# Optimization experiments

Measured on AMD Instinct MI355X. Metric: run time of the kernel, lower is better.

Reference implementation:

```python
import jax, jax.numpy as jnp
import numpy as np


def conv2d(x, w, b):
    # x: [D, Cin, H, W], w: [Cout, Cin, kh, kw], SAME padding, stride 1
    y = jax.lax.conv_general_dilated(
        x, w, window_strides=(1, 1), padding='SAME',
        dimension_numbers=('NCHW', 'OIHW', 'NCHW'))
    return y + b[None, :, None, None]


def setup_inputs() -> dict:
    key = jax.random.key(0)
    ks = jax.random.split(key, 12)
    B, N, T, H, W = 2, 3, 16, 28, 28
    Cp, Ch, Ck, Cv, Cs = 1024, 512, 64, 512, 256
    s = 0.02
    return {
        'f16': jax.random.normal(ks[0], (B, Cp, H, W), jnp.float32),
        'mk':  jax.random.normal(ks[1], (B, Ck, T, H, W), jnp.float32),
        'mv':  jax.random.normal(ks[2], (B, N, Cv, T, H, W), jnp.float32),
        'h':   jax.random.normal(ks[3], (B, N, Cs, H, W), jnp.float32),
        # KeyProj: 1x1 conv then 3x3 conv
        'w1': jax.random.normal(ks[4], (Ch, Cp, 1, 1), jnp.float32) * s,
        'b1': jnp.zeros((Ch,), jnp.float32),
        'w2': jax.random.normal(ks[5], (Ck, Ch, 3, 3), jnp.float32) * s,
        'b2': jnp.zeros((Ck,), jnp.float32),
        # sensory-updater transform: 3x3 conv, (Cv+Cs) -> 3*Cs
        'wt': jax.random.normal(ks[6], (3 * Cs, Cv + Cs, 3, 3), jnp.float32) * s,
        'bt': jnp.zeros((3 * Cs,), jnp.float32),
    }


def reference(f16, mk, mv, h, w1, b1, w2, b2, wt, bt):
    B, Ck, T = mk.shape[0], mk.shape[1], mk.shape[2]
    N, Cv = mv.shape[1], mv.shape[2]
    Cs = h.shape[2]
    H, W = f16.shape[-2:]
    P = H * W          # query pixels
    M = T * H * W      # memory slots

    # KeyProj: query key from pixel feature
    qk = conv2d(conv2d(f16, w1, b1), w2, b2)          # [B, Ck, H, W]

    # KV-memory affinity read (softmax over memory axis)
    mk_flat = mk.reshape(B, Ck, M)
    qk_flat = qk.reshape(B, Ck, P)
    logits = jnp.einsum('bcm,bcp->bmp', mk_flat, qk_flat) / jnp.sqrt(
        jnp.asarray(Ck, qk.dtype))                     # [B, M, P]
    aff = jax.nn.softmax(logits, axis=1)               # normalize over memory
    readout = jnp.einsum('bncm,bmp->bncp', mv.reshape(B, N, Cv, M), aff)
    readout = readout.reshape(B, N, Cv, H, W)          # [B, N, Cv, H, W]

    # gated recurrent sensory update (recurrent_update)
    x = jnp.concatenate([readout, h], axis=2).reshape(B * N, Cv + Cs, H, W)
    vals = conv2d(x, wt, bt).reshape(B, N, 3 * Cs, H, W)
    forget_g = jax.nn.sigmoid(vals[:, :, :Cs])
    update_g = jax.nn.sigmoid(vals[:, :, Cs:2 * Cs])
    new_vals = jnp.tanh(vals[:, :, 2 * Cs:])
    new_h = forget_g * h * (1.0 - update_g) + update_g * new_vals
    return new_h
```

## Files before the change

### kernel.cpp

```cpp
#include <hip/hip_runtime.h>

typedef unsigned short u16;
typedef unsigned int u32;
typedef float f32x4v __attribute__((ext_vector_type(4)));
typedef __bf16 bf16x8 __attribute__((ext_vector_type(8)));

#define GAS __attribute__((address_space(1)))
#define LAS __attribute__((address_space(3)))

__device__ __forceinline__ u16 f2bf(float f) {
  u32 u = __builtin_bit_cast(u32, f);
  u32 r = (u + 0x7FFFu + ((u >> 16) & 1u)) >> 16;
  return (u16)r;
}
__device__ __forceinline__ float bf2f(u16 h) {
  return __builtin_bit_cast(float, (u32)h << 16);
}
__device__ __forceinline__ void gld_lds16(const void* g, void* l) {
  __builtin_amdgcn_global_load_lds((const GAS void*)g, (LAS void*)l, 16, 0, 0);
}
#define VMCNT(N) asm volatile("s_waitcnt vmcnt(" #N ")" ::: "memory")
#define MFMA16(a, b, c) __builtin_amdgcn_mfma_f32_16x16x32_bf16((a), (b), (c), 0, 0, 0)

template <int CONV>
__device__ __forceinline__ void gemm8p_dev(
    int lb, int Gpad, const u16* A, const u16* B, u16* Cp,
    int M, int N, int Kc, int fullK, int S,
    long strA, long strB, long strC, int Cin, int gx, int gy, int nwg, u16* smem)
{
  const int cpx = Gpad >> 3;
  const int L = (lb & 7) * cpx + (lb >> 3);
  if (L >= nwg) return;
  const int by = L % gy;
  const int rest = L / gy;
  const int bx = rest % gx;
  const int z = rest / gx;

  const int t = threadIdx.x, lane = t & 63, wave = t >> 6;
  const int zb = z / S, s = z - zb * S;
  const int m0 = bx * 256, n0 = by * 256;
  const int kbeg = s * Kc;
  const int kavail = fullK - kbeg;
  const int kc = Kc < kavail ? Kc : kavail;
  const int T = kc >> 6;

  const int srow = t >> 3;
  const int g = ((t & 7) - (srow & 7)) & 7;
  const int ldsoff = t * 8;

  const u16* Asrc[2][2];
  #pragma unroll
  for (int h = 0; h < 2; ++h)
    #pragma unroll
    for (int q = 0; q < 2; ++q) {
      int r = m0 + h * 128 + q * 64 + srow; if (r >= M) r = M - 1;
      Asrc[h][q] = A + (long)zb * strA + (long)r * fullK + kbeg + g * 8;
    }
  const u16* Bsrc[2][2];
  #pragma unroll
  for (int h = 0; h < 2; ++h)
    #pragma unroll
    for (int q = 0; q < 2; ++q) {
      if constexpr (CONV) {
        int pn = n0 + h * 128 + q * 64 + srow; if (pn >= N) pn = 0;
        const int img = pn / 784, p = pn - img * 784;
        const int py = p / 28, px = p - py * 28;
        Bsrc[h][q] = B + ((long)img * 900 + (py + 1) * 30 + (px + 1)) * Cin + g * 8;
      } else {
        int r = n0 + h * 128 + q * 64 + srow; if (r >= N) r = N - 1;
        Bsrc[h][q] = B + (long)zb * strB + (long)r * fullK + kbeg + g * 8;
      }
    }

  auto stageA = [&](int tile, int h) {
    u16* d = smem + (((tile & 1) * 2 + h) * 8192);
    const long ko = (long)tile * 64;
    gld_lds16(Asrc[h][0] + ko, d + ldsoff);
    gld_lds16(Asrc[h][1] + ko, d + 4096 + ldsoff);
  };
  auto stageB = [&](int tile, int h) {
    u16* d = smem + 32768 + (((tile & 1) * 2 + h) * 8192);
    long off;
    if constexpr (CONV) {
      const int kg = kbeg + tile * 64;
      const int tap = kg / Cin, kc2 = kg - tap * Cin;
      off = (long)((tap / 3 - 1) * 30 + (tap % 3 - 1)) * Cin + kc2;
    } else {
      off = (long)tile * 64;
    }
    gld_lds16(Bsrc[h][0] + off, d + ldsoff);
    gld_lds16(Bsrc[h][1] + off, d + 4096 + ldsoff);
  };

  const int wm = wave & 1, wn = wave >> 1;
  const int lr = lane & 15, hi = lane >> 4;
  const int slot0 = ((hi + (lr & 7)) & 7) * 8;
  const int slot1 = (((hi + 4) + (lr & 7)) & 7) * 8;
  f32x4v acc[8][4] = {};
  bf16x8 breg[4][2];

  stageB(0, 0); stageB(0, 1);
  stageA(0, 0); stageA(0, 1);
  stageB(1, 0); stageB(1, 1);
  VMCNT(4);
  __builtin_amdgcn_s_barrier();

  for (int tau = 0; tau < T; ++tau) {
    const int d = tau & 1;
    const u16* aB = smem + ((d * 2 + wm) * 8192);
    const u16* bB = smem + 32768 + ((d * 2 + (wn >> 1)) * 8192);
    const int ta = (tau + 1 < T) ? tau + 1 : T - 1;
    const int tb = (tau + 2 < T) ? tau + 2 : T - 1;
    #pragma unroll
    for (int Q = 0; Q < 4; ++Q) {
      bf16x8 aph[2][2];
      #pragma unroll
      for (int m2 = 0; m2 < 2; ++m2) {
        const int lrow = (Q * 2 + m2) * 16 + lr;
        aph[m2][0] = *(const bf16x8*)&aB[lrow * 64 + slot0];
        aph[m2][1] = *(const bf16x8*)&aB[lrow * 64 + slot1];
      }
      if (Q == 0) {
        #pragma unroll
        for (int n = 0; n < 4; ++n) {
          const int lrow = (wn & 1) * 64 + n * 16 + lr;
          breg[n][0] = *(const bf16x8*)&bB[lrow * 64 + slot0];
          breg[n][1] = *(const bf16x8*)&bB[lrow * 64 + slot1];
        }
      }
      if      (Q == 0) stageA(ta, 0);
      else if (Q == 1) stageA(ta, 1);
      else if (Q == 2) stageB(tb, 0);
      else             { stageB(tb, 1); VMCNT(4); }
      __builtin_amdgcn_sched_barrier(0);
      __builtin_amdgcn_s_barrier();
      __builtin_amdgcn_s_setprio(1);
      #pragma unroll
      for (int m2 = 0; m2 < 2; ++m2)
        #pragma unroll
        for (int n = 0; n < 4; ++n) {
          acc[Q * 2 + m2][n] = MFMA16(aph[m2][0], breg[n][0], acc[Q * 2 + m2][n]);
          acc[Q * 2 + m2][n] = MFMA16(aph[m2][1], breg[n][1], acc[Q * 2 + m2][n]);
        }
      __builtin_amdgcn_s_setprio(0);
      __builtin_amdgcn_sched_barrier(0);
      __builtin_amdgcn_s_barrier();
    }
  }
  VMCNT(0);

  u16* Co = Cp + (long)z * strC;
  #pragma unroll
  for (int m = 0; m < 8; ++m)
    #pragma unroll
    for (int r = 0; r < 4; ++r) {
      const int row = m0 + wm * 128 + m * 16 + hi * 4 + r;
      if (row >= M) continue;
      #pragma unroll
      for (int n = 0; n < 4; ++n) {
        const int col = n0 + wn * 64 + n * 16 + lr;
        if (col < N) Co[(long)row * N + col] = f2bf(acc[m][n][r]);
      }
    }
}

__device__ __forceinline__ void gemmRC_dev(
    int lb, int Gpad, const u16* A, const u16* B, u16* Cp,
    int M, int N, int Kc, int fullK, int S,
    long strA, long strB, long strC, int gx, int gy, int nwg, u16* smem)
{
  const int cpx = Gpad >> 3;
  const int L = (lb & 7) * cpx + (lb >> 3);
  if (L >= nwg) return;
  const int by = L % gy;
  const int rest = L / gy;
  const int bx = rest % gx;
  const int z = rest / gx;

  u16* sA = smem;
  u16* sB = smem + 3 * 8192;
  const int t = threadIdx.x, lane = t & 63, wave = t >> 6;
  const int zb = z / S, s = z - zb * S;
  const int m0 = bx * 256, n0 = by * 128;
  const int kbeg = s * Kc;
  const int niter = Kc >> 5;

  const int schunk = ((t & 3) ^ ((t >> 4) & 3)) * 8;
  const u16* Ap[2]; const u16* Bp;
  #pragma unroll
  for (int q = 0; q < 2; ++q) {
    int ra = m0 + q * 128 + (t >> 2); if (ra >= M) ra = M - 1;
    Ap[q] = A + (long)zb * strA + (long)ra * fullK + schunk;
  }
  {
    int rb = n0 + (t >> 2); if (rb >= N) rb = N - 1;
    Bp = B + (long)zb * strB + (long)rb * fullK + schunk;
  }
  const int ldst = t * 8;

  auto stage = [&](int buf, int kg) {
    u16* dA = sA + buf * 8192;
    gld_lds16(Ap[0] + kg, &dA[ldst]);
    gld_lds16(Ap[1] + kg, &dA[4096 + ldst]);
    gld_lds16(Bp + kg,    &sB[buf * 4096 + ldst]);
  };

  const int wrow = (wave & 3) * 64, wcol = (wave >> 2) * 64;
  const int lr = lane & 15, hi = lane >> 4;
  const int csw = (hi ^ (lr >> 2)) * 8;
  f32x4v acc[4][4] = {};

  for (int p = 0; p < 2 && p < niter; ++p) stage(p, kbeg + p * 32);
  int cur = 0, nxt = 2;
  for (int it = 0; it < niter; ++it) {
    if (it + 2 < niter) {
      stage(nxt, kbeg + (it + 2) * 32);
      VMCNT(6);
    } else {
      const int rem = niter - 1 - it;
      if (rem == 1) VMCNT(3); else VMCNT(0);
    }
    __builtin_amdgcn_s_barrier();
    __builtin_amdgcn_sched_barrier(0);
    const u16* cA = sA + cur * 8192;
    const u16* cB = sB + cur * 4096;
    bf16x8 af[4], bf[4];
    #pragma unroll
    for (int m = 0; m < 4; ++m) af[m] = *(const bf16x8*)&cA[(wrow + m*16 + lr) * 32 + csw];
    #pragma unroll
    for (int n = 0; n < 4; ++n) bf[n] = *(const bf16x8*)&cB[(wcol + n*16 + lr) * 32 + csw];
    __builtin_amdgcn_s_setprio(1);
    #pragma unroll
    for (int m = 0; m < 4; ++m)
      #pragma unroll
      for (int n = 0; n < 4; ++n)
        acc[m][n] = MFMA16(af[m], bf[n], acc[m][n]);
    __builtin_amdgcn_s_setprio(0);
    __builtin_amdgcn_sched_barrier(0);
    __builtin_amdgcn_s_barrier();
    cur = (cur + 1 == 3) ? 0 : cur + 1;
    nxt = (nxt + 1 == 3) ? 0 : nxt + 1;
  }

  u16* Co = Cp + (long)z * strC;
  const int lq = hi * 4;
  #pragma unroll
  for (int m = 0; m < 4; ++m)
    #pragma unroll
    for (int r = 0; r < 4; ++r) {
      const int row = m0 + wrow + m * 16 + lq + r;
      if (row >= M) continue;
      #pragma unroll
      for (int n = 0; n < 4; ++n) {
        const int col = n0 + wcol + n * 16 + lr;
        if (col < N) Co[(long)row * N + col] = f2bf(acc[m][n][r]);
      }
    }
}

__device__ __forceinline__ void border_slot(int slot, int& py, int& px) {
  if (slot < 30)      { py = 0;         px = slot; }
  else if (slot < 60) { py = 29;        px = slot - 30; }
  else if (slot < 88) { py = slot - 59; px = 0; }
  else                { py = slot - 87; px = 29; }
}

__device__ __forceinline__ void transp_dev(
    const float* in, u16* out, int R, int C, int ldOut,
    int bx, int by, int t, float (*tile)[33])
{
  const int c0 = bx * 32, r0 = by * 32;
  const int tx = t & 31, ty = t >> 5;
  for (int i = ty; i < 32; i += 8) {
    const int r = r0 + i, c = c0 + tx;
    tile[i][tx] = (r < R && c < C) ? in[(long)r * C + c] : 0.0f;
  }
  __syncthreads();
  for (int i = ty; i < 32; i += 8) {
    const int r = r0 + tx, c = c0 + i;
    if (c < C && r < R)
      out[(long)c * ldOut + r] = f2bf(tile[tx][i]);
  }
}

__global__ __launch_bounds__(256) void prep1(
    const float* __restrict__ f16, const float* __restrict__ mk,
    const float* __restrict__ w1,
    u16* __restrict__ f16T, u16* __restrict__ mkT, u16* __restrict__ w1b)
{
  __shared__ float tile[32][33];
  const int bid = blockIdx.x, t = threadIdx.x;
  if (bid < 1600) {
    const int bx = bid % 25, by = (bid / 25) % 32, bz = bid / 800;
    transp_dev(f16 + (long)bz * 1024 * 784, f16T + (long)bz * 784 * 1024,
               1024, 784, 1024, bx, by, t, tile);
    return;
  }
  if (bid < 3168) {
    const int lb = bid - 1600;
    const int bx = lb % 392, by = (lb / 392) % 2, bz = lb / 784;
    transp_dev(mk + (long)bz * 64 * 12544, mkT + (long)bz * 12544 * 64,
               64, 12544, 64, bx, by, t, tile);
    return;
  }
  const long i = (long)(bid - 3168) * 256 + t;
  const float4* p = (const float4*)w1 + i * 2;
  const float4 a = p[0], b = p[1];
  u16 o[8] = {f2bf(a.x), f2bf(a.y), f2bf(a.z), f2bf(a.w),
              f2bf(b.x), f2bf(b.y), f2bf(b.z), f2bf(b.w)};
  ((uint4*)w1b)[i] = *(uint4*)o;
}

__global__ __launch_bounds__(512, 4) void fused1(
    const u16* __restrict__ f16T, const u16* __restrict__ w1b, u16* __restrict__ parts,
    const float* __restrict__ mv, u16* __restrict__ mvb,
    const float* __restrict__ w2, u16* __restrict__ w2R,
    const float* __restrict__ wt, u16* __restrict__ wtR,
    u16* __restrict__ out1P)
{
  extern __shared__ u16 smem[];
  const int bid = blockIdx.x, t = threadIdx.x;
  if (bid < 224) {
    gemmRC_dev(bid, 224, f16T, w1b, parts, 1568, 512, 128, 1024, 8,
               0, 0, 1568L * 512, 7, 4, 224, smem);
    return;
  }
  int lb = bid - 224;
  if (lb < 4704) {
    const long g0 = (long)lb * 1024 + t;
    #pragma unroll
    for (int k = 0; k < 2; ++k) {
      const long g = g0 + k * 512;
      const float4* p = (const float4*)mv + g * 2;
      const float4 a = p[0], b = p[1];
      u16 o[8] = {f2bf(a.x), f2bf(a.y), f2bf(a.z), f2bf(a.w),
                  f2bf(b.x), f2bf(b.y), f2bf(b.z), f2bf(b.w)};
      ((uint4*)mvb)[g] = *(uint4*)o;
    }
    return;
  }
  lb -= 4704;
  if (lb < 576) {
    const int idx = lb * 512 + t;
    const int c = idx % 512, tap = (idx / 512) % 9, m = idx / 4608;
    w2R[idx] = f2bf(w2[((long)m * 512 + c) * 9 + tap]);
    return;
  }
  lb -= 576;
  if (lb < 10368) {
    const long idx = (long)lb * 512 + t;
    const int c = (int)(idx % 768), tap = (int)((idx / 768) % 9), m = (int)(idx / 6912);
    wtR[idx] = f2bf(wt[((long)m * 768 + c) * 9 + tap]);
    return;
  }
  lb -= 10368;
  const int gid = lb * 512 + t;
  if (gid < 14848) {
    const int c8 = gid & 63, rest = gid >> 6;
    const int slot = rest % 116, img = rest / 116;
    int py, px; border_slot(slot, py, px);
    *(uint4*)&out1P[((long)img * 900 + py * 30 + px) * 512 + c8 * 8] =
        make_uint4(0, 0, 0, 0);
  }
}

template <int BK>
__global__ __launch_bounds__(256) void gemm_glds(
    const u16* __restrict__ A, const u16* __restrict__ B, u16* __restrict__ C,
    int M, int N, int Kc, int fullK, int S,
    long strA, long strB, long strC, float scale)
{
  constexpr int CPR = BK / 8;
  constexpr int ISS = BK / 16;
  __shared__ u16 sA[2][128 * BK];
  __shared__ u16 sB[2][128 * BK];
  const int t = threadIdx.x, lane = t & 63, wave = t >> 6;
  const int z = blockIdx.z, zb = z / S;
  const int m0 = blockIdx.x * 128, n0 = blockIdx.y * 128;
  const int kbeg = (z - zb * S) * Kc;

  const u16* Aptr[ISS]; const u16* Bptr[ISS]; int lofs[ISS];
  #pragma unroll
  for (int i = 0; i < ISS; ++i) {
    const int tp = i * 256 + t;
    const int r = tp / CPR;
    int c16 = tp % CPR;
    if constexpr (BK == 32) c16 = c16 ^ ((tp >> 4) & 3);
    else                    c16 = (c16 - (r & 7)) & 7;
    int ra = m0 + r; if (ra >= M) ra = M - 1;
    int rb = n0 + r; if (rb >= N) rb = N - 1;
    Aptr[i] = A + (long)zb * strA + (long)ra * fullK + kbeg + c16 * 8;
    Bptr[i] = B + (long)zb * strB + (long)rb * fullK + kbeg + c16 * 8;
    lofs[i] = (i * 256 + (wave << 6)) * 8;
  }
  auto stage = [&](int buf, int k0) {
    #pragma unroll
    for (int i = 0; i < ISS; ++i) {
      gld_lds16(Aptr[i] + k0, &sA[buf][lofs[i]]);
      gld_lds16(Bptr[i] + k0, &sB[buf][lofs[i]]);
    }
  };

  const int wr = (wave >> 1) * 64, wc = (wave & 1) * 64;
  const int lr = lane & 15, hi = lane >> 4;
  f32x4v acc[4][4] = {};
  const int niter = Kc / BK;

  stage(0, 0);
  for (int it = 0; it < niter; ++it) {
    const int cur = it & 1;
    if (it + 1 < niter) {
      stage(cur ^ 1, (it + 1) * BK);
      if constexpr (ISS == 2) VMCNT(4); else VMCNT(8);
    } else {
      VMCNT(0);
    }
    __builtin_amdgcn_s_barrier();
    __builtin_amdgcn_sched_barrier(0);
    #pragma unroll
    for (int kk = 0; kk < BK; kk += 32) {
      bf16x8 af[4], bv[4];
      #pragma unroll
      for (int i = 0; i < 4; ++i) {
        const int row = wr + i*16 + lr;
        int lk;
        if constexpr (BK == 32) lk = kk + ((hi ^ (lr >> 2)) * 8);
        else                    lk = ((((kk >> 3) + hi) + (row & 7)) & 7) * 8;
        af[i] = *(const bf16x8*)&sA[cur][row * BK + lk];
      }
      #pragma unroll
      for (int j = 0; j < 4; ++j) {
        const int row = wc + j*16 + lr;
        int lk;
        if constexpr (BK == 32) lk = kk + ((hi ^ (lr >> 2)) * 8);
        else                    lk = ((((kk >> 3) + hi) + (row & 7)) & 7) * 8;
        bv[j] = *(const bf16x8*)&sB[cur][row * BK + lk];
      }
      __builtin_amdgcn_s_setprio(1);
      #pragma unroll
      for (int i = 0; i < 4; ++i)
        #pragma unroll
        for (int j = 0; j < 4; ++j)
          acc[i][j] = MFMA16(af[i], bv[j], acc[i][j]);
      __builtin_amdgcn_s_setprio(0);
    }
    __builtin_amdgcn_sched_barrier(0);
    __builtin_amdgcn_s_barrier();
  }

  const int lq = hi * 4;
  u16* Cw = C + (long)zb * strC;
  #pragma unroll
  for (int i = 0; i < 4; ++i)
    #pragma unroll
    for (int r = 0; r < 4; ++r) {
      const int row = m0 + wr + i*16 + lq + r;
      if (row >= M) continue;
      #pragma unroll
      for (int j = 0; j < 4; ++j) {
        const int col = n0 + wc + j*16 + lr;
        if (col < N) Cw[(long)row * N + col] = f2bf(acc[i][j][r] * scale);
      }
    }
}

__global__ __launch_bounds__(256) void conv_glds(
    const u16* __restrict__ Wt, const u16* __restrict__ imgP,
    float* __restrict__ Cp, int M, int Cin, int Ntot, int Kc)
{
  __shared__ u16 sA[2][128 * 32];
  __shared__ u16 sB[2][128 * 32];
  const int t = threadIdx.x, lane = t & 63, wave = t >> 6;
  const int z = blockIdx.z;
  const int m0 = blockIdx.x * 128, n0 = blockIdx.y * 128;
  const int kbeg = z * Kc;

  const u16* Aptr[2]; const u16* Bptr[2]; int lofs[2];
  #pragma unroll
  for (int i = 0; i < 2; ++i) {
    const int tp = i * 256 + t;
    const int r = tp >> 2;
    const int c16 = (tp & 3) ^ ((tp >> 4) & 3);
    int ra = m0 + r; if (ra >= M) ra = M - 1;
    int pn = n0 + r; if (pn >= Ntot) pn = 0;
    const int img = pn / 784, p = pn - img * 784;
    const int py = p / 28, px = p - py * 28;
    Aptr[i] = Wt + (long)ra * (9 * Cin) + c16 * 8;
    Bptr[i] = imgP + ((long)img * 900 + (py + 1) * 30 + (px + 1)) * Cin + c16 * 8;
    lofs[i] = (i * 256 + (wave << 6)) * 8;
  }
  auto stage = [&](int buf, int kg) {
    const int tap = kg / Cin, kc = kg - tap * Cin;
    const long off = (long)((tap / 3 - 1) * 30 + (tap % 3 - 1)) * Cin + kc;
    #pragma unroll
    for (int i = 0; i < 2; ++i) {
      gld_lds16(Aptr[i] + kg, &sA[buf][lofs[i]]);
      gld_lds16(Bptr[i] + off, &sB[buf][lofs[i]]);
    }
  };

  const int wr = (wave >> 1) * 64, wc = (wave & 1) * 64;
  const int lr = lane & 15, hi = lane >> 4;
  const int csw = (hi ^ (lr >> 2)) * 8;
  f32x4v acc[4][4] = {};
  const int niter = Kc >> 5;

  stage(0, kbeg);
  for (int it = 0; it < niter; ++it) {
    const int cur = it & 1;
    if (it + 1 < niter) {
      stage(cur ^ 1, kbeg + (it + 1) * 32);
      VMCNT(4);
    } else {
      VMCNT(0);
    }
    __builtin_amdgcn_s_barrier();
    __builtin_amdgcn_sched_barrier(0);
    bf16x8 af[4], bv[4];
    #pragma unroll
    for (int i = 0; i < 4; ++i) af[i] = *(const bf16x8*)&sA[cur][(wr + i*16 + lr) * 32 + csw];
    #pragma unroll
    for (int j = 0; j < 4; ++j) bv[j] = *(const bf16x8*)&sB[cur][(wc + j*16 + lr) * 32 + csw];
    __builtin_amdgcn_s_setprio(1);
    #pragma unroll
    for (int i = 0; i < 4; ++i)
      #pragma unroll
      for (int j = 0; j < 4; ++j)
        acc[i][j] = MFMA16(af[i], bv[j], acc[i][j]);
    __builtin_amdgcn_s_setprio(0);
    __builtin_amdgcn_sched_barrier(0);
    __builtin_amdgcn_s_barrier();
  }

  float* Co = Cp + (long)z * M * Ntot;
  const int lq = hi * 4;
  #pragma unroll
  for (int i = 0; i < 4; ++i)
    #pragma unroll
    for (int r = 0; r < 4; ++r) {
      const int row = m0 + wr + i*16 + lq + r;
      if (row >= M) continue;
      #pragma unroll
      for (int j = 0; j < 4; ++j) {
        const int col = n0 + wc + j*16 + lr;
        if (col < Ntot) Co[(long)row * Ntot + col] = acc[i][j][r];
      }
    }
}

__device__ __forceinline__ void addbf4(float* a, uint2 v) {
  a[0] += bf2f((u16)(v.x & 0xFFFFu));
  a[1] += bf2f((u16)(v.x >> 16));
  a[2] += bf2f((u16)(v.y & 0xFFFFu));
  a[3] += bf2f((u16)(v.y >> 16));
}

__global__ __launch_bounds__(256) void reduce_c1_bf(
    const u16* __restrict__ parts, u16* __restrict__ dst,
    const float* __restrict__ bias, int S)
{
  const long idx = (long)blockIdx.x * 256 + threadIdx.x;
  if (idx >= 1568L * 128) return;
  const int c4 = (int)(idx & 127), p = (int)(idx >> 7);
  const int c = c4 * 4;
  float sum[4] = {bias[c], bias[c+1], bias[c+2], bias[c+3]};
  for (int s = 0; s < S; ++s)
    addbf4(sum, *(const uint2*)&parts[((long)s * 1568 + p) * 512 + c]);
  const int im = p / 784, q = p - im * 784;
  const int qpad = (q / 28 + 1) * 30 + (q % 28 + 1);
  u16 o[4] = {f2bf(sum[0]), f2bf(sum[1]), f2bf(sum[2]), f2bf(sum[3])};
  *(uint2*)&dst[((long)im * 900 + qpad) * 512 + c] = *(uint2*)o;
}

__global__ __launch_bounds__(256) void reduceT_ro(
    const u16* __restrict__ parts, u16* __restrict__ dst, int S)
{
  __shared__ float tile[32][33];
  const int b = blockIdx.z, c0 = blockIdx.x * 32, p0 = blockIdx.y * 32;
  const int tx = threadIdx.x & 31, ty = threadIdx.x >> 5;
  for (int i = ty; i < 32; i += 8) {
    const int pc = min(p0 + tx, 783);
    float s = 0;
    for (int k = 0; k < S; ++k)
      s += bf2f(parts[((long)(b * S + k) * 1536 + c0 + i) * 784 + pc]);
    tile[i][tx] = s;
  }
  __syncthreads();
  for (int i = ty; i < 32; i += 8) {
    const int p = p0 + i, c = c0 + tx;
    if (p < 784) {
      const int n = c >> 9, cc = c & 511;
      const int qpad = (p / 28 + 1) * 30 + (p % 28 + 1);
      dst[((long)(b * 3 + n) * 900 + qpad) * 768 + cc] = f2bf(tile[tx][i]);
    }
  }
}

__global__ __launch_bounds__(256) void reduceT_qk(
    const float* __restrict__ parts, u16* __restrict__ dst,
    const float* __restrict__ bias, int S)
{
  __shared__ float tile[32][33];
  const int b = blockIdx.z, c0 = blockIdx.x * 32, p0 = blockIdx.y * 32;
  const int tx = threadIdx.x & 31, ty = threadIdx.x >> 5;
  for (int i = ty; i < 32; i += 8) {
    const int pc = min(p0 + tx, 783);
    const long base = (long)(c0 + i) * 1568 + b * 784 + pc;
    float s = 0;
    for (int k = 0; k < S; ++k) s += parts[(long)k * 64 * 1568 + base];
    tile[i][tx] = s;
  }
  __syncthreads();
  for (int i = ty; i < 32; i += 8) {
    const int p = p0 + i, c = c0 + tx;
    if (p < 784)
      dst[((long)b * 784 + p) * 64 + c] = f2bf(tile[tx][i] + bias[c]);
  }
}

__global__ __launch_bounds__(256) void softmax_inplace(u16* __restrict__ buf)
{
  uint4* p4 = (uint4*)(buf + (long)blockIdx.x * 12544);
  const int t = threadIdx.x;
  __shared__ float red[4];
  uint4 v[7];
  float mx = -3.0e38f;
  #pragma unroll
  for (int q = 0; q < 7; ++q) {
    const int idx = t + q * 256;
    if (idx < 1568) {
      v[q] = p4[idx];
      const u32 w[4] = {v[q].x, v[q].y, v[q].z, v[q].w};
      #pragma unroll
      for (int e = 0; e < 4; ++e) {
        mx = fmaxf(mx, bf2f((u16)(w[e] & 0xFFFFu)));
        mx = fmaxf(mx, bf2f((u16)(w[e] >> 16)));
      }
    }
  }
  #pragma unroll
  for (int o = 32; o > 0; o >>= 1) mx = fmaxf(mx, __shfl_xor(mx, o));
  if ((t & 63) == 0) red[t >> 6] = mx;
  __syncthreads();
  mx = fmaxf(fmaxf(red[0], red[1]), fmaxf(red[2], red[3]));

  float s = 0.0f;
  #pragma unroll
  for (int q = 0; q < 7; ++q) {
    const int idx = t + q * 256;
    if (idx < 1568) {
      const u32 w[4] = {v[q].x, v[q].y, v[q].z, v[q].w};
      #pragma unroll
      for (int e = 0; e < 4; ++e) {
        s += __expf(bf2f((u16)(w[e] & 0xFFFFu)) - mx);
        s += __expf(bf2f((u16)(w[e] >> 16)) - mx);
      }
    }
  }
  #pragma unroll
  for (int o = 32; o > 0; o >>= 1) s += __shfl_xor(s, o);
  __syncthreads();
  if ((t & 63) == 0) red[t >> 6] = s;
  __syncthreads();
  const float inv = 1.0f / (red[0] + red[1] + red[2] + red[3]);

  #pragma unroll
  for (int q = 0; q < 7; ++q) {
    const int idx = t + q * 256;
    if (idx < 1568) {
      u32 w[4] = {v[q].x, v[q].y, v[q].z, v[q].w};
      #pragma unroll
      for (int e = 0; e < 4; ++e) {
        const float a = __expf(bf2f((u16)(w[e] & 0xFFFFu)) - mx) * inv;
        const float b = __expf(bf2f((u16)(w[e] >> 16)) - mx) * inv;
        w[e] = (u32)f2bf(a) | ((u32)f2bf(b) << 16);
      }
      p4[idx] = make_uint4(w[0], w[1], w[2], w[3]);
    }
  }
}

__global__ __launch_bounds__(512, 2) void fused_ro(
    const u16* __restrict__ mvb, const u16* __restrict__ logaff,
    u16* __restrict__ parts, const float* __restrict__ hin,
    u16* __restrict__ concatP, int Kc, int S)
{
  extern __shared__ u16 smem[];
  const int bid = blockIdx.x, t = threadIdx.x;
  if (bid < 240) {
    gemm8p_dev<0>(bid, 240, mvb, logaff, parts, 1536, 784, Kc, 12544, S,
                  1536L * 12544, 784L * 12544, 1536L * 784, 0, 6, 4, 240, smem);
    return;
  }
  int lb = bid - 240;
  if (lb < 1200) {
    float (*tile)[33] = (float(*)[33])smem;
    const int bx = lb % 8, by = (lb / 8) % 25, zimg = lb / 200;
    const int c0 = bx * 32, p0 = by * 32;
    const int tx = t & 31, ty = t >> 5;
    for (int i = ty; i < 32; i += 16) {
      const int pc = min(p0 + tx, 783);
      tile[i][tx] = hin[((long)zimg * 256 + c0 + i) * 784 + pc];
    }
    __syncthreads();
    for (int i = ty; i < 32; i += 16) {
      const int p = p0 + i, c = c0 + tx;
      if (p < 784) {
        const int qpad = (p / 28 + 1) * 30 + (p % 28 + 1);
        concatP[((long)zimg * 900 + qpad) * 768 + 512 + c] = f2bf(tile[tx][i]);
      }
    }
    return;
  }
  lb -= 1200;
  const int gid = lb * 512 + t;
  if (gid < 66816) {
    const int c8 = gid % 96, rest = gid / 96;
    const int slot = rest % 116, img = rest / 116;
    int py, px; border_slot(slot, py, px);
    *(uint4*)&concatP[((long)img * 900 + py * 30 + px) * 768 + c8 * 8] =
        make_uint4(0, 0, 0, 0);
  }
}

__global__ __launch_bounds__(512, 2) void gemm8p_tr(
    const u16* __restrict__ A, const u16* __restrict__ B, u16* __restrict__ Cp,
    int M, int N, int Kc, int fullK, int S,
    long strC, int Cin, int gx, int gy, int nwg)
{
  extern __shared__ u16 smem[];
  gemm8p_dev<1>(blockIdx.x, (int)gridDim.x, A, B, Cp, M, N, Kc, fullK, S,
                0, 0, strC, Cin, gx, gy, nwg, smem);
}

__global__ __launch_bounds__(256) void treduce_gate(
    const u16* __restrict__ parts, const float* __restrict__ bt,
    const float* __restrict__ h, float* __restrict__ out, int S)
{
  const long i = (long)blockIdx.x * 256 + threadIdx.x;
  if (i >= 6L * 256 * 196) return;
  const int p4 = (int)(i % 196);
  const int rest = (int)(i / 196);
  const int cs = rest % 256, im = rest / 256;
  const long slice = 768L * 4704;
  const long pbase = (long)im * 784 + p4 * 4;
  float F[4] = {}, U[4] = {}, NV[4] = {};
  for (int s = 0; s < S; ++s) {
    const u16* P = parts + (long)s * slice;
    addbf4(F,  *(const uint2*)&P[(long)cs         * 4704 + pbase]);
    addbf4(U,  *(const uint2*)&P[(long)(256 + cs) * 4704 + pbase]);
    addbf4(NV, *(const uint2*)&P[(long)(512 + cs) * 4704 + pbase]);
  }
  const float bF = bt[cs], bU = bt[256 + cs], bN = bt[512 + cs];
  const f32x4v hv = ((const f32x4v*)h)[((long)(im * 256 + cs) * 784 >> 2) + p4];
  f32x4v o;
  #pragma unroll
  for (int q = 0; q < 4; ++q) {
    const float f = F[q] + bF, u = U[q] + bU, nv = NV[q] + bN;
    const float sf = 1.0f / (1.0f + __expf(-f));
    const float su = 1.0f / (1.0f + __expf(-u));
    const float e2 = __expf(2.0f * nv);
    const float tv = (e2 - 1.0f) / (e2 + 1.0f);
    o[q] = sf * hv[q] * (1.0f - su) + su * tv;
  }
  ((f32x4v*)out)[((long)(im * 256 + cs) * 784 >> 2) + p4] = o;
}

__global__ __launch_bounds__(256) void fill_sentinel(float* p, long n) {
  const long i = (long)blockIdx.x * 256 + threadIdx.x;
  if (i < n) p[i] = 12345.0f;
}

extern "C" void kernel_launch(void* const* d_in, const int* in_sizes, int n_in,
                              void* d_out, int out_size, void* d_ws, size_t ws_size,
                              hipStream_t stream) {
  const float* f16 = (const float*)d_in[0];
  const float* mk  = (const float*)d_in[1];
  const float* mv  = (const float*)d_in[2];
  const float* hin = (const float*)d_in[3];
  const float* w1  = (const float*)d_in[4];
  const float* b1  = (const float*)d_in[5];
  const float* w2  = (const float*)d_in[6];
  const float* b2  = (const float*)d_in[7];
  const float* wt  = (const float*)d_in[8];
  const float* bt  = (const float*)d_in[9];
  float* out = (float*)d_out;

  (void)hipFuncSetAttribute((const void*)fused1,
                            hipFuncAttributeMaxDynamicSharedMemorySize, 73728);
  (void)hipFuncSetAttribute((const void*)fused_ro,
                            hipFuncAttributeMaxDynamicSharedMemorySize, 131072);
  (void)hipFuncSetAttribute((const void*)gemm8p_tr,
                            hipFuncAttributeMaxDynamicSharedMemorySize, 131072);
  constexpr unsigned DSMR = 73728, DSM8 = 131072;

  const size_t B_f16T   = 2UL*784*1024*2;
  const size_t B_w1b    = 512UL*1024*2;
  const size_t B_w2R    = 64UL*4608*2;
  const size_t B_out1P  = 2UL*900*512*2;
  const size_t B_qkT    = 2UL*784*64*2;
  const size_t B_concat = 6UL*900*768*2;
  const size_t B_wtR    = 768UL*6912*2;
  const size_t B_mkT    = 2UL*12544*64*2;
  const size_t B_logaff = 2UL*784*12544*2;
  const size_t B_mvb    = 38535168UL*2;
  auto al = [](size_t x) { return (x + 255) & ~(size_t)255; };

  const size_t phase1 = al(B_f16T) + al(B_w1b) + al(B_w2R) + al(B_out1P) + al(B_qkT);
  const size_t regionA = phase1 > al(B_concat) ? phase1 : al(B_concat);

  const int S_ro = 5, S_tr = 4, S_c1 = 8;
  const int Kc_ro = 2560, Kc_tr = 1728;
  auto poolBytes = [&]() -> size_t {
    size_t p2 = 18UL*64*1568*4;
    size_t p1 = (size_t)S_c1*1568*512*2;
    size_t pr = (size_t)(2*S_ro)*1536*784*2;
    size_t pt = (size_t)S_tr*768*4704*2;
    size_t m = p2; if (p1 > m) m = p1; if (pr > m) m = pr; if (pt > m) m = pt;
    return m;
  };
  const size_t fixed = regionA + al(B_wtR) + al(B_mkT) + al(B_logaff) + al(B_mvb);
  if (fixed + poolBytes() > ws_size) {
    fill_sentinel<<<4704, 256, 0, stream>>>(out, (long)out_size);
    return;
  }

  char* base = (char*)d_ws;
  size_t off = 0;
  auto alloc = [&](size_t bytes) -> char* { char* p = base + off; off += al(bytes); return p; };
  char* rA = alloc(regionA);
  u16* f16T   = (u16*)rA;
  u16* w1b    = (u16*)(rA + al(B_f16T));
  u16* w2R    = (u16*)(rA + al(B_f16T) + al(B_w1b));
  u16* out1P  = (u16*)(rA + al(B_f16T) + al(B_w1b) + al(B_w2R));
  u16* qkT    = (u16*)(rA + al(B_f16T) + al(B_w1b) + al(B_w2R) + al(B_out1P));
  u16* concatP = (u16*)rA;
  u16*   wtR     = (u16*)alloc(B_wtR);
  u16*   mkT     = (u16*)alloc(B_mkT);
  u16*   logaff  = (u16*)alloc(B_logaff);
  u16*   mvb     = (u16*)alloc(B_mvb);
  char*  partsRaw = alloc(poolBytes());
  float* partsF  = (float*)partsRaw;
  u16*   partsH  = (u16*)partsRaw;

  prep1<<<3424, 256, 0, stream>>>(f16, mk, w1, f16T, mkT, w1b);

  fused1<<<15901, 512, DSMR, stream>>>(f16T, w1b, partsH, mv, mvb,
                                       w2, w2R, wt, wtR, out1P);

  reduce_c1_bf<<<784, 256, 0, stream>>>(partsH, out1P, b1, S_c1);

  conv_glds<<<dim3(1, 13, 18), 256, 0, stream>>>(w2R, out1P, partsF, 64, 512, 1568, 256);

  reduceT_qk<<<dim3(2, 25, 2), 256, 0, stream>>>(partsF, qkT, b2, 18);

  gemm_glds<64><<<dim3(7, 98, 2), 256, 0, stream>>>(
      qkT, mkT, logaff, 784, 12544, 64, 64, 1,
      784L*64, 12544L*64, 784L*12544, 0.125f);

  softmax_inplace<<<1568, 256, 0, stream>>>(logaff);

  fused_ro<<<1571, 512, DSM8, stream>>>(mvb, logaff, partsH, hin, concatP,
                                        Kc_ro, S_ro);

  reduceT_ro<<<dim3(48, 25, 2), 256, 0, stream>>>(partsH, concatP, S_ro);

  gemm8p_tr<<<232, 512, DSM8, stream>>>(wtR, concatP, partsH,
                                        768, 4704, Kc_tr, 6912, S_tr,
                                        768L*4704, 768, 3, 19, 228);

  treduce_gate<<<1176, 256, 0, stream>>>(partsH, bt, hin, out, S_tr);
}
```

Before: 305.8 us.

## Rebalance conversion work across kernels to overlap with conv and GEMM

Moves the w2/wt weight reorder-and-convert out of fused1 into prep1, and moves the large mv fp32-to-bf16 conversion into a new conv2_mv kernel that runs it alongside the small 3x3 conv GEMM. fused1 now holds only the 1x1 conv GEMM and border zeroing, so its GEMM blocks no longer share the launch with thousands of elementwise blocks. The aim is to fill idle CUs during the underoccupied conv (234 blocks) with bandwidth-bound conversion work. The risk is that the conversion blocks compete with the conv for bandwidth, and prep1 gets larger.

```diff
diff --git a/kernel.cpp b/kernel.cpp
--- a/kernel.cpp
+++ b/kernel.cpp
@@ -285,8 +285,10 @@
 
 __global__ __launch_bounds__(256) void prep1(
     const float* __restrict__ f16, const float* __restrict__ mk,
-    const float* __restrict__ w1,
-    u16* __restrict__ f16T, u16* __restrict__ mkT, u16* __restrict__ w1b)
+    const float* __restrict__ w1, const float* __restrict__ w2,
+    const float* __restrict__ wt,
+    u16* __restrict__ f16T, u16* __restrict__ mkT, u16* __restrict__ w1b,
+    u16* __restrict__ w2R, u16* __restrict__ wtR)
 {
   __shared__ float tile[32][33];
   const int bid = blockIdx.x, t = threadIdx.x;
@@ -303,20 +305,29 @@
                64, 12544, 64, bx, by, t, tile);
     return;
   }
-  const long i = (long)(bid - 3168) * 256 + t;
-  const float4* p = (const float4*)w1 + i * 2;
-  const float4 a = p[0], b = p[1];
-  u16 o[8] = {f2bf(a.x), f2bf(a.y), f2bf(a.z), f2bf(a.w),
-              f2bf(b.x), f2bf(b.y), f2bf(b.z), f2bf(b.w)};
-  ((uint4*)w1b)[i] = *(uint4*)o;
+  if (bid < 3424) {
+    const long i = (long)(bid - 3168) * 256 + t;
+    const float4* p = (const float4*)w1 + i * 2;
+    const float4 a = p[0], b = p[1];
+    u16 o[8] = {f2bf(a.x), f2bf(a.y), f2bf(a.z), f2bf(a.w),
+                f2bf(b.x), f2bf(b.y), f2bf(b.z), f2bf(b.w)};
+    ((uint4*)w1b)[i] = *(uint4*)o;
+    return;
+  }
+  if (bid < 4576) {
+    const int idx = (bid - 3424) * 256 + t;
+    const int c = idx % 512, tap = (idx / 512) % 9, m = idx / 4608;
+    w2R[idx] = f2bf(w2[((long)m * 512 + c) * 9 + tap]);
+    return;
+  }
+  const long idx = (long)(bid - 4576) * 256 + t;
+  const int c = (int)(idx % 768), tap = (int)((idx / 768) % 9), m = (int)(idx / 6912);
+  wtR[idx] = f2bf(wt[((long)m * 768 + c) * 9 + tap]);
 }
 
 __global__ __launch_bounds__(512, 4) void fused1(
-    const u16* __restrict__ f16T, const u16* __restrict__ w1b, u16* __restrict__ parts,
-    const float* __restrict__ mv, u16* __restrict__ mvb,
-    const float* __restrict__ w2, u16* __restrict__ w2R,
-    const float* __restrict__ wt, u16* __restrict__ wtR,
-    u16* __restrict__ out1P)
+    const u16* __restrict__ f16T, const u16* __restrict__ w1b,
+    u16* __restrict__ parts, u16* __restrict__ out1P)
 {
   extern __shared__ u16 smem[];
   const int bid = blockIdx.x, t = threadIdx.x;
@@ -325,36 +336,7 @@
                0, 0, 1568L * 512, 7, 4, 224, smem);
     return;
   }
-  int lb = bid - 224;
-  if (lb < 4704) {
-    const long g0 = (long)lb * 1024 + t;
-    #pragma unroll
-    for (int k = 0; k < 2; ++k) {
-      const long g = g0 + k * 512;
-      const float4* p = (const float4*)mv + g * 2;
-      const float4 a = p[0], b = p[1];
-      u16 o[8] = {f2bf(a.x), f2bf(a.y), f2bf(a.z), f2bf(a.w),
-                  f2bf(b.x), f2bf(b.y), f2bf(b.z), f2bf(b.w)};
-      ((uint4*)mvb)[g] = *(uint4*)o;
-    }
-    return;
-  }
-  lb -= 4704;
-  if (lb < 576) {
-    const int idx = lb * 512 + t;
-    const int c = idx % 512, tap = (idx / 512) % 9, m = idx / 4608;
-    w2R[idx] = f2bf(w2[((long)m * 512 + c) * 9 + tap]);
-    return;
-  }
-  lb -= 576;
-  if (lb < 10368) {
-    const long idx = (long)lb * 512 + t;
-    const int c = (int)(idx % 768), tap = (int)((idx / 768) % 9), m = (int)(idx / 6912);
-    wtR[idx] = f2bf(wt[((long)m * 768 + c) * 9 + tap]);
-    return;
-  }
-  lb -= 10368;
-  const int gid = lb * 512 + t;
+  const int gid = (bid - 224) * 512 + t;
   if (gid < 14848) {
     const int c8 = gid & 63, rest = gid >> 6;
     const int slot = rest % 116, img = rest / 116;
@@ -362,6 +344,102 @@
     *(uint4*)&out1P[((long)img * 900 + py * 30 + px) * 512 + c8 * 8] =
         make_uint4(0, 0, 0, 0);
   }
+}
+
+__global__ __launch_bounds__(256) void conv2_mv(
+    const u16* __restrict__ Wt, const u16* __restrict__ imgP,
+    float* __restrict__ Cp, const float* __restrict__ mv, u16* __restrict__ mvb)
+{
+  __shared__ u16 sA[2][128 * 32];
+  __shared__ u16 sB[2][128 * 32];
+  const int bid = blockIdx.x, t = threadIdx.x;
+  if (bid >= 234) {
+    for (long g = (long)(bid - 234) * 256 + t; g < 4816896L; g += 2048L * 256) {
+      const float4* p = (const float4*)mv + g * 2;
+      const float4 a = p[0], b = p[1];
+      u16 o[8] = {f2bf(a.x), f2bf(a.y), f2bf(a.z), f2bf(a.w),
+                  f2bf(b.x), f2bf(b.y), f2bf(b.z), f2bf(b.w)};
+      ((uint4*)mvb)[g] = *(uint4*)o;
+    }
+    return;
+  }
+  const int lane = t & 63, wave = t >> 6;
+  const int z = bid / 13;
+  const int m0 = 0, n0 = (bid % 13) * 128;
+  const int Cin = 512, Ntot = 1568, M = 64, Kc = 256;
+  const int kbeg = z * Kc;
+
+  const u16* Aptr[2]; const u16* Bptr[2]; int lofs[2];
+  #pragma unroll
+  for (int i = 0; i < 2; ++i) {
+    const int tp = i * 256 + t;
+    const int r = tp >> 2;
+    const int c16 = (tp & 3) ^ ((tp >> 4) & 3);
+    int ra = m0 + r; if (ra >= M) ra = M - 1;
+    int pn = n0 + r; if (pn >= Ntot) pn = 0;
+    const int img = pn / 784, p = pn - img * 784;
+    const int py = p / 28, px = p - py * 28;
+    Aptr[i] = Wt + (long)ra * (9 * Cin) + c16 * 8;
+    Bptr[i] = imgP + ((long)img * 900 + (py + 1) * 30 + (px + 1)) * Cin + c16 * 8;
+    lofs[i] = (i * 256 + (wave << 6)) * 8;
+  }
+  auto stage = [&](int buf, int kg) {
+    const int tap = kg / Cin, kc = kg - tap * Cin;
+    const long off = (long)((tap / 3 - 1) * 30 + (tap % 3 - 1)) * Cin + kc;
+    #pragma unroll
+    for (int i = 0; i < 2; ++i) {
+      gld_lds16(Aptr[i] + kg, &sA[buf][lofs[i]]);
+      gld_lds16(Bptr[i] + off, &sB[buf][lofs[i]]);
+    }
+  };
+
+  const int wr = (wave >> 1) * 64, wc = (wave & 1) * 64;
+  const int lr = lane & 15, hi = lane >> 4;
+  const int csw = (hi ^ (lr >> 2)) * 8;
+  f32x4v acc[4][4] = {};
+  const int niter = Kc >> 5;
+
+  stage(0, kbeg);
+  for (int it = 0; it < niter; ++it) {
+    const int cur = it & 1;
+    if (it + 1 < niter) {
+      stage(cur ^ 1, kbeg + (it + 1) * 32);
+      VMCNT(4);
+    } else {
+      VMCNT(0);
+    }
+    __builtin_amdgcn_s_barrier();
+    __builtin_amdgcn_sched_barrier(0);
+    bf16x8 af[4], bv[4];
+    #pragma unroll
+    for (int i = 0; i < 4; ++i) af[i] = *(const bf16x8*)&sA[cur][(wr + i*16 + lr) * 32 + csw];
+    #pragma unroll
+    for (int j = 0; j < 4; ++j) bv[j] = *(const bf16x8*)&sB[cur][(wc + j*16 + lr) * 32 + csw];
+    __builtin_amdgcn_s_setprio(1);
+    #pragma unroll
+    for (int i = 0; i < 4; ++i)
+      #pragma unroll
+      for (int j = 0; j < 4; ++j)
+        acc[i][j] = MFMA16(af[i], bv[j], acc[i][j]);
+    __builtin_amdgcn_s_setprio(0);
+    __builtin_amdgcn_sched_barrier(0);
+    __builtin_amdgcn_s_barrier();
+  }
+
+  float* Co = Cp + (long)z * M * Ntot;
+  const int lq = hi * 4;
+  #pragma unroll
+  for (int i = 0; i < 4; ++i)
+    #pragma unroll
+    for (int r = 0; r < 4; ++r) {
+      const int row = m0 + wr + i*16 + lq + r;
+      if (row >= M) continue;
+      #pragma unroll
+      for (int j = 0; j < 4; ++j) {
+        const int col = n0 + wc + j*16 + lr;
+        if (col < Ntot) Co[(long)row * Ntot + col] = acc[i][j][r];
+      }
+    }
 }
 
 template <int BK>
@@ -460,90 +538,6 @@
       for (int j = 0; j < 4; ++j) {
         const int col = n0 + wc + j*16 + lr;
         if (col < N) Cw[(long)row * N + col] = f2bf(acc[i][j][r] * scale);
-      }
-    }
-}
-
-__global__ __launch_bounds__(256) void conv_glds(
-    const u16* __restrict__ Wt, const u16* __restrict__ imgP,
-    float* __restrict__ Cp, int M, int Cin, int Ntot, int Kc)
-{
-  __shared__ u16 sA[2][128 * 32];
-  __shared__ u16 sB[2][128 * 32];
-  const int t = threadIdx.x, lane = t & 63, wave = t >> 6;
-  const int z = blockIdx.z;
-  const int m0 = blockIdx.x * 128, n0 = blockIdx.y * 128;
-  const int kbeg = z * Kc;
-
-  const u16* Aptr[2]; const u16* Bptr[2]; int lofs[2];
-  #pragma unroll
-  for (int i = 0; i < 2; ++i) {
-    const int tp = i * 256 + t;
-    const int r = tp >> 2;
-    const int c16 = (tp & 3) ^ ((tp >> 4) & 3);
-    int ra = m0 + r; if (ra >= M) ra = M - 1;
-    int pn = n0 + r; if (pn >= Ntot) pn = 0;
-    const int img = pn / 784, p = pn - img * 784;
-    const int py = p / 28, px = p - py * 28;
-    Aptr[i] = Wt + (long)ra * (9 * Cin) + c16 * 8;
-    Bptr[i] = imgP + ((long)img * 900 + (py + 1) * 30 + (px + 1)) * Cin + c16 * 8;
-    lofs[i] = (i * 256 + (wave << 6)) * 8;
-  }
-  auto stage = [&](int buf, int kg) {
-    const int tap = kg / Cin, kc = kg - tap * Cin;
-    const long off = (long)((tap / 3 - 1) * 30 + (tap % 3 - 1)) * Cin + kc;
-    #pragma unroll
-    for (int i = 0; i < 2; ++i) {
-      gld_lds16(Aptr[i] + kg, &sA[buf][lofs[i]]);
-      gld_lds16(Bptr[i] + off, &sB[buf][lofs[i]]);
-    }
-  };
-
-  const int wr = (wave >> 1) * 64, wc = (wave & 1) * 64;
-  const int lr = lane & 15, hi = lane >> 4;
-  const int csw = (hi ^ (lr >> 2)) * 8;
-  f32x4v acc[4][4] = {};
-  const int niter = Kc >> 5;
-
-  stage(0, kbeg);
-  for (int it = 0; it < niter; ++it) {
-    const int cur = it & 1;
-    if (it + 1 < niter) {
-      stage(cur ^ 1, kbeg + (it + 1) * 32);
-      VMCNT(4);
-    } else {
-      VMCNT(0);
-    }
-    __builtin_amdgcn_s_barrier();
-    __builtin_amdgcn_sched_barrier(0);
-    bf16x8 af[4], bv[4];
-    #pragma unroll
-    for (int i = 0; i < 4; ++i) af[i] = *(const bf16x8*)&sA[cur][(wr + i*16 + lr) * 32 + csw];
-    #pragma unroll
-    for (int j = 0; j < 4; ++j) bv[j] = *(const bf16x8*)&sB[cur][(wc + j*16 + lr) * 32 + csw];
-    __builtin_amdgcn_s_setprio(1);
-    #pragma unroll
-    for (int i = 0; i < 4; ++i)
-      #pragma unroll
-      for (int j = 0; j < 4; ++j)
-        acc[i][j] = MFMA16(af[i], bv[j], acc[i][j]);
-    __builtin_amdgcn_s_setprio(0);
-    __builtin_amdgcn_sched_barrier(0);
-    __builtin_amdgcn_s_barrier();
-  }
-
-  float* Co = Cp + (long)z * M * Ntot;
-  const int lq = hi * 4;
-  #pragma unroll
-  for (int i = 0; i < 4; ++i)
-    #pragma unroll
-    for (int r = 0; r < 4; ++r) {
-      const int row = m0 + wr + i*16 + lq + r;
-      if (row >= M) continue;
-      #pragma unroll
-      for (int j = 0; j < 4; ++j) {
-        const int col = n0 + wc + j*16 + lr;
-        if (col < Ntot) Co[(long)row * Ntot + col] = acc[i][j][r];
       }
     }
 }
@@ -843,14 +837,13 @@
   float* partsF  = (float*)partsRaw;
   u16*   partsH  = (u16*)partsRaw;
 
-  prep1<<<3424, 256, 0, stream>>>(f16, mk, w1, f16T, mkT, w1b);
-
-  fused1<<<15901, 512, DSMR, stream>>>(f16T, w1b, partsH, mv, mvb,
-                                       w2, w2R, wt, wtR, out1P);
+  prep1<<<25312, 256, 0, stream>>>(f16, mk, w1, w2, wt, f16T, mkT, w1b, w2R, wtR);
+
+  fused1<<<253, 512, DSMR, stream>>>(f16T, w1b, partsH, out1P);
 
   reduce_c1_bf<<<784, 256, 0, stream>>>(partsH, out1P, b1, S_c1);
 
-  conv_glds<<<dim3(1, 13, 18), 256, 0, stream>>>(w2R, out1P, partsF, 64, 512, 1568, 256);
+  conv2_mv<<<2282, 256, 0, stream>>>(w2R, out1P, partsF, mv, mvb);
 
   reduceT_qk<<<dim3(2, 25, 2), 256, 0, stream>>>(partsF, qkT, b2, 18);
 
```

Result: no change. 300.0 us (-1.9%).
